# Performance work log

Hardware: AMD Instinct MI355X
Metric: run time of the kernel (lower is better)

## Reference

```python
import jax, jax.numpy as jnp
import numpy as np


def _morpho(x, weight, bias, sign, padding, stride):
    # x: [B,C,H,W], weight: [B,C,kh,kw], bias: [B,C], sign: [B]
    B, C, H, W = x.shape
    kh, kw = weight.shape[-2:]
    # sign handling: if |sign| >= 1e-7 multiply by sign, else leave unchanged
    m = (jnp.abs(sign) >= 1e-7).astype(x.dtype)          # [B], constant (detached in torch)
    s = m * sign + (1.0 - m)                              # effective multiplier per sample
    xs = x * s[:, None, None, None]
    # unfold zero-pads, and sign*0 == 0, so padding signed x with zeros is equivalent
    xp = jnp.pad(xs, ((0, 0), (0, 0), (padding, padding), (padding, padding)))
    H2 = (H + 2 * padding - kh) // stride + 1
    W2 = (W + 2 * padding - kw) // stride + 1
    # direct windowed max-plus: y[b,c,i,j] = max_{p,q} xs_pad[b,c,i*s+p,j*s+q] + w[b,c,p,q]
    # small fixed kh*kw loop avoids materializing the B*C*kh*kw*L unfold tensor
    y = jnp.full((B, C, H2, W2), -jnp.inf, dtype=x.dtype)
    for p in range(kh):
        for q in range(kw):
            patch = jax.lax.slice(
                xp,
                (0, 0, p, q),
                (B, C, p + (H2 - 1) * stride + 1, q + (W2 - 1) * stride + 1),
                (1, 1, stride, stride),
            )  # [B,C,H2,W2]
            y = jnp.maximum(y, patch + weight[:, :, p, q][:, :, None, None])
    y = y + bias[:, :, None, None]
    return y * s[:, None, None, None]


def setup_inputs() -> dict:
    key = jax.random.key(0)
    k1, k2, k3, k4 = jax.random.split(key, 4)
    B, C, H, W, kh, kw = 16, 64, 128, 128, 5, 5
    return {
        "x": jax.random.normal(k1, (B, C, H, W), dtype=jnp.float32),
        "weight": jax.random.normal(k2, (B, C, kh, kw), dtype=jnp.float32) * 0.1,
        "bias": jax.random.normal(k3, (B, C), dtype=jnp.float32) * 0.1,
        "sign": jax.random.normal(k4, (B,), dtype=jnp.float32),
        "padding": 2,
        "stride": 1,
    }


def reference(x, weight, bias, sign, padding, stride):
    return _morpho(x, weight, bias, sign, padding, stride)
```

## Files before the change

kernel.cpp:

```cpp
#include <hip/hip_runtime.h>
#include <math.h>
#include <stdint.h>

#define HH 128
#define WW 128

typedef __fp16 h2 __attribute__((ext_vector_type(2)));

__device__ __forceinline__ h2 h2max(h2 a, h2 b) { return __builtin_elementwise_max(a, b); }
__device__ __forceinline__ uint32_t h2u(h2 v) { return __builtin_bit_cast(uint32_t, v); }
__device__ __forceinline__ h2 uh2(uint32_t v) { return __builtin_bit_cast(h2, v); }

#if __has_builtin(__builtin_elementwise_fma)
#define H2FMA(a, b, c) __builtin_elementwise_fma((a), (b), (c))
#else
#define H2FMA(a, b, c) ((a) * (b) + (c))
#endif

#define WAITV(n) do { asm volatile("s_waitcnt vmcnt(" #n ")" ::: "memory"); \
                      __builtin_amdgcn_sched_barrier(0); } while (0)

__global__ __launch_bounds__(256) void morpho_kernel(
    const float* __restrict__ x,
    const float* __restrict__ wgt,
    const float* __restrict__ bias,
    const float* __restrict__ sign,
    float* __restrict__ out)
{
    const int bid  = blockIdx.x;
    const int blk  = (bid & 7) * 512 + (bid >> 3);
    const int quad = blk & 3;
    const int bc   = blk >> 2;
    const int b    = bc >> 6;

    float*       __restrict__ yp = out + (size_t)bc * (HH * WW);
    const float* __restrict__ wp = wgt + bc * 25;

    const float sgn = sign[b];
    const float s   = (fabsf(sgn) >= 1e-7f) ? sgn : 1.0f;
    const float bvs = bias[bc] * s;
    const __fp16 sh = (__fp16)s;
    const h2 s2 = { sh, sh };

    uint32_t wsu[25];
#pragma unroll
    for (int k = 0; k < 25; ++k) {
        const __fp16 wh = (__fp16)wp[k];
        h2 w2 = { wh, wh };
        wsu[k] = (uint32_t)__builtin_amdgcn_readfirstlane((int)h2u(w2));
    }

    const int t  = threadIdx.x;
    const int tx = t & 31;
    const int ty = t >> 5;
    const int j0 = tx * 4;
    const int i0 = quad * 32 + ty * 4;
    const int planeOff = bc * (HH * WW);
    const bool mL = (tx > 0);
    const bool mR = (tx < 31);

    asm volatile("s_waitcnt vmcnt(0)" ::: "memory");

    float4 vm[8];
#pragma unroll
    for (int r8 = 0; r8 < 8; ++r8) {
        const int rrow = i0 - 2 + r8;
        const int rc   = min(max(rrow, 0), HH - 1);
        const float* gp = x + planeOff + rc * WW + j0;
        asm volatile("global_load_dwordx4 %0, %1, off" : "=v"(vm[r8]) : "v"(gp));
    }

    h2 acc0[4], acc1[4];

#pragma unroll
    for (int r8 = 0; r8 < 8; ++r8) {
        switch (7 - r8) {
            case 7: WAITV(7); break;
            case 6: WAITV(6); break;
            case 5: WAITV(5); break;
            case 4: WAITV(4); break;
            case 3: WAITV(3); break;
            case 2: WAITV(2); break;
            case 1: WAITV(1); break;
            default: WAITV(0); break;
        }
        const int  rrow = i0 - 2 + r8;
        const bool rv = ((unsigned)rrow < (unsigned)HH);
        uint32_t e1 = h2u(__builtin_amdgcn_cvt_pkrtz(vm[r8].x, vm[r8].y));
        uint32_t e2 = h2u(__builtin_amdgcn_cvt_pkrtz(vm[r8].z, vm[r8].w));
        e1 = rv ? e1 : 0u;
        e2 = rv ? e2 : 0u;
        uint32_t e0 = (uint32_t)__shfl_up((int)e2, 1, 32);
        uint32_t e3 = (uint32_t)__shfl_down((int)e1, 1, 32);
        e0 = mL ? e0 : 0u;
        e3 = mR ? e3 : 0u;
        const uint32_t o0 = __builtin_amdgcn_alignbit(e1, e0, 16);
        const uint32_t o1 = __builtin_amdgcn_alignbit(e2, e1, 16);
        const uint32_t o2 = __builtin_amdgcn_alignbit(e3, e2, 16);
        const uint32_t P0[5] = { e0, o0, e1, o1, e2 };
        const uint32_t P1[5] = { e1, o1, e2, o2, e3 };

#pragma unroll
        for (int p = 0; p < 5; ++p) {
            const int oi = r8 - p;
            if (oi >= 0 && oi < 4) {
                const h2 w0 = uh2(wsu[p * 5 + 0]);
                const h2 w1 = uh2(wsu[p * 5 + 1]);
                const h2 w2 = uh2(wsu[p * 5 + 2]);
                const h2 w3 = uh2(wsu[p * 5 + 3]);
                const h2 w4 = uh2(wsu[p * 5 + 4]);
                {
                    const h2 t0 = H2FMA(uh2(P0[0]), s2, w0);
                    const h2 t1 = H2FMA(uh2(P0[1]), s2, w1);
                    const h2 t2 = H2FMA(uh2(P0[2]), s2, w2);
                    const h2 t3 = H2FMA(uh2(P0[3]), s2, w3);
                    const h2 t4 = H2FMA(uh2(P0[4]), s2, w4);
                    h2 mm = h2max(h2max(h2max(t0, t1), h2max(t2, t3)), t4);
                    acc0[oi] = (p == 0) ? mm : h2max(acc0[oi], mm);
                }
                {
                    const h2 t0 = H2FMA(uh2(P1[0]), s2, w0);
                    const h2 t1 = H2FMA(uh2(P1[1]), s2, w1);
                    const h2 t2 = H2FMA(uh2(P1[2]), s2, w2);
                    const h2 t3 = H2FMA(uh2(P1[3]), s2, w3);
                    const h2 t4 = H2FMA(uh2(P1[4]), s2, w4);
                    h2 mm = h2max(h2max(h2max(t0, t1), h2max(t2, t3)), t4);
                    acc1[oi] = (p == 0) ? mm : h2max(acc1[oi], mm);
                }
            }
        }
    }

#pragma unroll
    for (int a = 0; a < 4; ++a) {
        float4 o;
        o.x = fmaf((float)acc0[a][0], s, bvs);
        o.y = fmaf((float)acc0[a][1], s, bvs);
        o.z = fmaf((float)acc1[a][0], s, bvs);
        o.w = fmaf((float)acc1[a][1], s, bvs);
        *reinterpret_cast<float4*>(yp + (size_t)(i0 + a) * WW + j0) = o;
    }
}

extern "C" void kernel_launch(void* const* d_in, const int* in_sizes, int n_in,
                              void* d_out, int out_size, void* d_ws, size_t ws_size,
                              hipStream_t stream) {
    (void)d_ws; (void)ws_size; (void)in_sizes; (void)n_in; (void)out_size;
    const float* x    = (const float*)d_in[0];
    const float* w    = (const float*)d_in[1];
    const float* bias = (const float*)d_in[2];
    const float* sign = (const float*)d_in[3];
    float* out = (float*)d_out;

    morpho_kernel<<<4096, 256, 0, stream>>>(x, w, bias, sign, out);
}
```

Before: 27.93 us.

## Process a whole plane per block with rolling cross-quad load pipelining

Each block now handles all four 32-row quads of one (b,c) plane instead of one quad, and the grid shrinks from 4096 to 1024 blocks. Loads for the next quad's rows are issued right after each row of the current quad is consumed. This keeps eight row loads in flight through the whole plane and spreads the weight-conversion setup over more work. The cost is fewer resident waves to hide latency. On this target stores also count toward vmcnt, so the fixed vmcnt(7) waits after each store batch may stall longer than needed.

Measured after the change: 27.48 us. About the same (-1.6%).

```diff
diff --git a/kernel.cpp b/kernel.cpp
--- a/kernel.cpp
+++ b/kernel.cpp
@@ -27,11 +27,9 @@
     const float* __restrict__ sign,
     float* __restrict__ out)
 {
-    const int bid  = blockIdx.x;
-    const int blk  = (bid & 7) * 512 + (bid >> 3);
-    const int quad = blk & 3;
-    const int bc   = blk >> 2;
-    const int b    = bc >> 6;
+    const int bid = blockIdx.x;
+    const int bc  = (bid & 7) * 128 + (bid >> 3);
+    const int b   = bc >> 6;
 
     float*       __restrict__ yp = out + (size_t)bc * (HH * WW);
     const float* __restrict__ wp = wgt + bc * 25;
@@ -54,38 +52,24 @@
     const int tx = t & 31;
     const int ty = t >> 5;
     const int j0 = tx * 4;
-    const int i0 = quad * 32 + ty * 4;
     const int planeOff = bc * (HH * WW);
     const bool mL = (tx > 0);
     const bool mR = (tx < 31);
 
-    asm volatile("s_waitcnt vmcnt(0)" ::: "memory");
+    float4 vm[8];
+    h2 acc0[4], acc1[4];
 
-    float4 vm[8];
-#pragma unroll
-    for (int r8 = 0; r8 < 8; ++r8) {
-        const int rrow = i0 - 2 + r8;
+    auto ISSUE = [&](int q, int r) {
+        const int rrow = q * 32 + ty * 4 - 2 + r;
         const int rc   = min(max(rrow, 0), HH - 1);
         const float* gp = x + planeOff + rc * WW + j0;
-        asm volatile("global_load_dwordx4 %0, %1, off" : "=v"(vm[r8]) : "v"(gp));
-    }
+        asm volatile("global_load_dwordx4 %0, %1, off" : "=v"(vm[r]) : "v"(gp));
+    };
 
-    h2 acc0[4], acc1[4];
-
-#pragma unroll
-    for (int r8 = 0; r8 < 8; ++r8) {
-        switch (7 - r8) {
-            case 7: WAITV(7); break;
-            case 6: WAITV(6); break;
-            case 5: WAITV(5); break;
-            case 4: WAITV(4); break;
-            case 3: WAITV(3); break;
-            case 2: WAITV(2); break;
-            case 1: WAITV(1); break;
-            default: WAITV(0); break;
-        }
+    auto CONSUME = [&](int q, int r8) {
+        const int  i0   = q * 32 + ty * 4;
         const int  rrow = i0 - 2 + r8;
-        const bool rv = ((unsigned)rrow < (unsigned)HH);
+        const bool rv   = ((unsigned)rrow < (unsigned)HH);
         uint32_t e1 = h2u(__builtin_amdgcn_cvt_pkrtz(vm[r8].x, vm[r8].y));
         uint32_t e2 = h2u(__builtin_amdgcn_cvt_pkrtz(vm[r8].z, vm[r8].w));
         e1 = rv ? e1 : 0u;
@@ -99,7 +83,6 @@
         const uint32_t o2 = __builtin_amdgcn_alignbit(e3, e2, 16);
         const uint32_t P0[5] = { e0, o0, e1, o1, e2 };
         const uint32_t P1[5] = { e1, o1, e2, o2, e3 };
-
 #pragma unroll
         for (int p = 0; p < 5; ++p) {
             const int oi = r8 - p;
@@ -129,17 +112,62 @@
                 }
             }
         }
-    }
+    };
 
+    auto STORE = [&](int q) {
+        const int i0 = q * 32 + ty * 4;
 #pragma unroll
-    for (int a = 0; a < 4; ++a) {
-        float4 o;
-        o.x = fmaf((float)acc0[a][0], s, bvs);
-        o.y = fmaf((float)acc0[a][1], s, bvs);
-        o.z = fmaf((float)acc1[a][0], s, bvs);
-        o.w = fmaf((float)acc1[a][1], s, bvs);
-        *reinterpret_cast<float4*>(yp + (size_t)(i0 + a) * WW + j0) = o;
-    }
+        for (int a = 0; a < 4; ++a) {
+            float4 o;
+            o.x = fmaf((float)acc0[a][0], s, bvs);
+            o.y = fmaf((float)acc0[a][1], s, bvs);
+            o.z = fmaf((float)acc1[a][0], s, bvs);
+            o.w = fmaf((float)acc1[a][1], s, bvs);
+            *reinterpret_cast<float4*>(yp + (size_t)(i0 + a) * WW + j0) = o;
+        }
+    };
+
+    asm volatile("s_waitcnt vmcnt(0)" ::: "memory");
+
+    ISSUE(0,0); ISSUE(0,1); ISSUE(0,2); ISSUE(0,3);
+    ISSUE(0,4); ISSUE(0,5); ISSUE(0,6); ISSUE(0,7);
+
+    WAITV(7); CONSUME(0,0); ISSUE(1,0);
+    WAITV(7); CONSUME(0,1); ISSUE(1,1);
+    WAITV(7); CONSUME(0,2); ISSUE(1,2);
+    WAITV(7); CONSUME(0,3); ISSUE(1,3);
+    WAITV(7); CONSUME(0,4); ISSUE(1,4);
+    WAITV(7); CONSUME(0,5); ISSUE(1,5);
+    WAITV(7); CONSUME(0,6); ISSUE(1,6);
+    WAITV(7); CONSUME(0,7); ISSUE(1,7);
+    STORE(0);
+    WAITV(7); CONSUME(1,0); ISSUE(2,0);
+    WAITV(7); CONSUME(1,1); ISSUE(2,1);
+    WAITV(7); CONSUME(1,2); ISSUE(2,2);
+    WAITV(7); CONSUME(1,3); ISSUE(2,3);
+    WAITV(7); CONSUME(1,4); ISSUE(2,4);
+    WAITV(7); CONSUME(1,5); ISSUE(2,5);
+    WAITV(7); CONSUME(1,6); ISSUE(2,6);
+    WAITV(7); CONSUME(1,7); ISSUE(2,7);
+    STORE(1);
+    WAITV(7); CONSUME(2,0); ISSUE(3,0);
+    WAITV(7); CONSUME(2,1); ISSUE(3,1);
+    WAITV(7); CONSUME(2,2); ISSUE(3,2);
+    WAITV(7); CONSUME(2,3); ISSUE(3,3);
+    WAITV(7); CONSUME(2,4); ISSUE(3,4);
+    WAITV(7); CONSUME(2,5); ISSUE(3,5);
+    WAITV(7); CONSUME(2,6); ISSUE(3,6);
+    WAITV(7); CONSUME(2,7); ISSUE(3,7);
+    STORE(2);
+    WAITV(7); CONSUME(3,0);
+    WAITV(6); CONSUME(3,1);
+    WAITV(5); CONSUME(3,2);
+    WAITV(4); CONSUME(3,3);
+    WAITV(3); CONSUME(3,4);
+    WAITV(2); CONSUME(3,5);
+    WAITV(1); CONSUME(3,6);
+    WAITV(0); CONSUME(3,7);
+    STORE(3);
 }
 
 extern "C" void kernel_launch(void* const* d_in, const int* in_sizes, int n_in,
@@ -152,5 +180,5 @@
     const float* sign = (const float*)d_in[3];
     float* out = (float*)d_out;
 
-    morpho_kernel<<<4096, 256, 0, stream>>>(x, w, bias, sign, out);
+    morpho_kernel<<<1024, 256, 0, stream>>>(x, w, bias, sign, out);
 }
```

## Process whole plane per block with rolling software-pipelined row loads

Applied to the files above, without the earlier changes.

Each block now covers a full 128x128 channel plane by walking its four 32-row quarters in sequence, so the grid shrinks from 4096 to 1024 blocks. Row loads for the next quarter are issued while the current quarter's rows are consumed, keeping about eight loads in flight, and output rows are stored as soon as they are complete. The aim is to hide load latency across quarters and cut per-block setup such as weight conversion and sign handling. In exchange there are fewer resident blocks, and the stores also count toward the vmcnt waits, which may make some waits stricter than intended.

Measured after the change: 27.31 us. 2.2% less time.

```diff
diff --git a/kernel.cpp b/kernel.cpp
--- a/kernel.cpp
+++ b/kernel.cpp
@@ -27,11 +27,9 @@
     const float* __restrict__ sign,
     float* __restrict__ out)
 {
-    const int bid  = blockIdx.x;
-    const int blk  = (bid & 7) * 512 + (bid >> 3);
-    const int quad = blk & 3;
-    const int bc   = blk >> 2;
-    const int b    = bc >> 6;
+    const int bid = blockIdx.x;
+    const int bc  = (bid & 7) * 128 + (bid >> 3);
+    const int b   = bc >> 6;
 
     float*       __restrict__ yp = out + (size_t)bc * (HH * WW);
     const float* __restrict__ wp = wgt + bc * 25;
@@ -50,46 +48,33 @@
         wsu[k] = (uint32_t)__builtin_amdgcn_readfirstlane((int)h2u(w2));
     }
 
-    const int t  = threadIdx.x;
-    const int tx = t & 31;
-    const int ty = t >> 5;
-    const int j0 = tx * 4;
-    const int i0 = quad * 32 + ty * 4;
-    const int planeOff = bc * (HH * WW);
+    const int t   = threadIdx.x;
+    const int tx  = t & 31;
+    const int ty4 = (t >> 5) * 4;
+    const int j0  = tx * 4;
+    const float* __restrict__ xcb = x + bc * (HH * WW) + j0;
     const bool mL = (tx > 0);
     const bool mR = (tx < 31);
 
-    asm volatile("s_waitcnt vmcnt(0)" ::: "memory");
-
     float4 vm[8];
-#pragma unroll
-    for (int r8 = 0; r8 < 8; ++r8) {
-        const int rrow = i0 - 2 + r8;
-        const int rc   = min(max(rrow, 0), HH - 1);
-        const float* gp = x + planeOff + rc * WW + j0;
-        asm volatile("global_load_dwordx4 %0, %1, off" : "=v"(vm[r8]) : "v"(gp));
-    }
-
     h2 acc0[4], acc1[4];
 
-#pragma unroll
-    for (int r8 = 0; r8 < 8; ++r8) {
-        switch (7 - r8) {
-            case 7: WAITV(7); break;
-            case 6: WAITV(6); break;
-            case 5: WAITV(5); break;
-            case 4: WAITV(4); break;
-            case 3: WAITV(3); break;
-            case 2: WAITV(2); break;
-            case 1: WAITV(1); break;
-            default: WAITV(0); break;
+    auto ISSUE = [&](int q, int r, bool clampRow) {
+        int rrow = q * 32 + ty4 - 2 + r;
+        if (clampRow) rrow = min(max(rrow, 0), HH - 1);
+        const float* gp = xcb + rrow * WW;
+        asm volatile("global_load_dwordx4 %0, %1, off" : "=v"(vm[r]) : "v"(gp));
+    };
+
+    auto CONSUME = [&](int q, int r8, bool rowmask) {
+        bool rv = true;
+        if (rowmask) {
+            const int rrow = q * 32 + ty4 - 2 + r8;
+            rv = ((unsigned)rrow < (unsigned)HH);
         }
-        const int  rrow = i0 - 2 + r8;
-        const bool rv = ((unsigned)rrow < (unsigned)HH);
         uint32_t e1 = h2u(__builtin_amdgcn_cvt_pkrtz(vm[r8].x, vm[r8].y));
         uint32_t e2 = h2u(__builtin_amdgcn_cvt_pkrtz(vm[r8].z, vm[r8].w));
-        e1 = rv ? e1 : 0u;
-        e2 = rv ? e2 : 0u;
+        if (rowmask) { e1 = rv ? e1 : 0u; e2 = rv ? e2 : 0u; }
         uint32_t e0 = (uint32_t)__shfl_up((int)e2, 1, 32);
         uint32_t e3 = (uint32_t)__shfl_down((int)e1, 1, 32);
         e0 = mL ? e0 : 0u;
@@ -99,7 +84,6 @@
         const uint32_t o2 = __builtin_amdgcn_alignbit(e3, e2, 16);
         const uint32_t P0[5] = { e0, o0, e1, o1, e2 };
         const uint32_t P1[5] = { e1, o1, e2, o2, e3 };
-
 #pragma unroll
         for (int p = 0; p < 5; ++p) {
             const int oi = r8 - p;
@@ -129,17 +113,55 @@
                 }
             }
         }
-    }
+    };
 
-#pragma unroll
-    for (int a = 0; a < 4; ++a) {
+    auto STORE_ROW = [&](int q, int a) {
         float4 o;
         o.x = fmaf((float)acc0[a][0], s, bvs);
         o.y = fmaf((float)acc0[a][1], s, bvs);
         o.z = fmaf((float)acc1[a][0], s, bvs);
         o.w = fmaf((float)acc1[a][1], s, bvs);
-        *reinterpret_cast<float4*>(yp + (size_t)(i0 + a) * WW + j0) = o;
-    }
+        *reinterpret_cast<float4*>(yp + (size_t)(q * 32 + ty4 + a) * WW + j0) = o;
+    };
+
+    asm volatile("s_waitcnt vmcnt(0)" ::: "memory");
+
+    ISSUE(0,0,true); ISSUE(0,1,true);
+    ISSUE(0,2,false); ISSUE(0,3,false); ISSUE(0,4,false);
+    ISSUE(0,5,false); ISSUE(0,6,false); ISSUE(0,7,false);
+
+    WAITV(7); CONSUME(0,0,true);  ISSUE(1,0,false);
+    WAITV(7); CONSUME(0,1,true);  ISSUE(1,1,false);
+    WAITV(7); CONSUME(0,2,false); ISSUE(1,2,false);
+    WAITV(7); CONSUME(0,3,false); ISSUE(1,3,false);
+    WAITV(7); CONSUME(0,4,false); ISSUE(1,4,false); STORE_ROW(0,0);
+    WAITV(7); CONSUME(0,5,false); ISSUE(1,5,false); STORE_ROW(0,1);
+    WAITV(7); CONSUME(0,6,false); ISSUE(1,6,false); STORE_ROW(0,2);
+    WAITV(7); CONSUME(0,7,false); ISSUE(1,7,false); STORE_ROW(0,3);
+    WAITV(7); CONSUME(1,0,false); ISSUE(2,0,false);
+    WAITV(7); CONSUME(1,1,false); ISSUE(2,1,false);
+    WAITV(7); CONSUME(1,2,false); ISSUE(2,2,false);
+    WAITV(7); CONSUME(1,3,false); ISSUE(2,3,false);
+    WAITV(7); CONSUME(1,4,false); ISSUE(2,4,false); STORE_ROW(1,0);
+    WAITV(7); CONSUME(1,5,false); ISSUE(2,5,false); STORE_ROW(1,1);
+    WAITV(7); CONSUME(1,6,false); ISSUE(2,6,false); STORE_ROW(1,2);
+    WAITV(7); CONSUME(1,7,false); ISSUE(2,7,false); STORE_ROW(1,3);
+    WAITV(7); CONSUME(2,0,false); ISSUE(3,0,false);
+    WAITV(7); CONSUME(2,1,false); ISSUE(3,1,false);
+    WAITV(7); CONSUME(2,2,false); ISSUE(3,2,false);
+    WAITV(7); CONSUME(2,3,false); ISSUE(3,3,false);
+    WAITV(7); CONSUME(2,4,false); ISSUE(3,4,false); STORE_ROW(2,0);
+    WAITV(7); CONSUME(2,5,false); ISSUE(3,5,false); STORE_ROW(2,1);
+    WAITV(7); CONSUME(2,6,false); ISSUE(3,6,true);  STORE_ROW(2,2);
+    WAITV(7); CONSUME(2,7,false); ISSUE(3,7,true);  STORE_ROW(2,3);
+    WAITV(7); CONSUME(3,0,false);
+    WAITV(6); CONSUME(3,1,false);
+    WAITV(5); CONSUME(3,2,false);
+    WAITV(4); CONSUME(3,3,false);
+    WAITV(3); CONSUME(3,4,false);                   STORE_ROW(3,0);
+    WAITV(2); CONSUME(3,5,false);                   STORE_ROW(3,1);
+    WAITV(1); CONSUME(3,6,true);                    STORE_ROW(3,2);
+    WAITV(0); CONSUME(3,7,true);                    STORE_ROW(3,3);
 }
 
 extern "C" void kernel_launch(void* const* d_in, const int* in_sizes, int n_in,
@@ -152,5 +174,5 @@
     const float* sign = (const float*)d_in[3];
     float* out = (float*)d_out;
 
-    morpho_kernel<<<4096, 256, 0, stream>>>(x, w, bias, sign, out);
+    morpho_kernel<<<1024, 256, 0, stream>>>(x, w, bias, sign, out);
 }
```
